# Kernel tuning notes

Hardware: AMD Instinct MI355X
Metric: run time of the kernel (lower is better)

The kernel has to match this reference:

```python
import jax, jax.numpy as jnp
import numpy as np

L = 16          # num transformer layers
D = 1024        # d_model
H = 16          # num heads
HD = 64         # head dim
LDIM = 512      # latent dim
TC = 512        # text conditioning length
PAST = 1024     # kv cache past length
FF = 4096       # ffn hidden
FH = 2048       # flow net hidden
MAX_PERIOD = 10000.0


def _ln(x, w, b, eps=1e-5):
    mu = jnp.mean(x, axis=-1, keepdims=True)
    var = jnp.mean((x - mu) ** 2, axis=-1, keepdims=True)
    return (x - mu) * jax.lax.rsqrt(var + eps) * w + b


def setup_inputs() -> dict:
    key = jax.random.key(0)
    ks = jax.random.split(key, 13)
    n = lambda k, s: jax.random.normal(k, s, dtype=jnp.float32)
    inp = {
        'text_embeddings': n(ks[0], (1, TC, D)),
        'prev_latent': n(ks[1], (1, 1, LDIM)),
        'kv_cache': n(ks[2], (L, 2, 1, PAST, H, HD)),
        'cache_len': PAST,
        'noise': n(ks[3], (1, LDIM)),
        'bos_emb': n(ks[4], (LDIM,)),
        'W_in': n(ks[5], (LDIM, D)) * 0.02, 'b_in': jnp.zeros((D,), jnp.float32),
        'ln1_w': jnp.ones((L, D), jnp.float32), 'ln1_b': jnp.zeros((L, D), jnp.float32),
        'Wqkv': n(ks[6], (L, D, 3 * D)) * 0.02, 'bqkv': jnp.zeros((L, 3 * D), jnp.float32),
        'Wo': n(ks[7], (L, D, D)) * 0.02, 'bo': jnp.zeros((L, D), jnp.float32),
        'ln2_w': jnp.ones((L, D), jnp.float32), 'ln2_b': jnp.zeros((L, D), jnp.float32),
        'W1': n(ks[8], (L, D, FF)) * 0.02, 'b1': jnp.zeros((L, FF), jnp.float32),
        'W2': n(ks[9], (L, FF, D)) * 0.02, 'b2': jnp.zeros((L, D), jnp.float32),
        'on_w': jnp.ones((D,), jnp.float32), 'on_b': jnp.zeros((D,), jnp.float32),
        'W_eos': n(ks[10], (D, 1)) * 0.02, 'b_eos': jnp.zeros((1,), jnp.float32),
        'Wf1': n(ks[11], (D + 2 + LDIM, FH)) * 0.02, 'bf1': jnp.zeros((FH,), jnp.float32),
        'Wf2': n(ks[12], (FH, LDIM)) * 0.02, 'bf2': jnp.zeros((LDIM,), jnp.float32),
    }
    return inp


def reference(text_embeddings, prev_latent, kv_cache, cache_len, noise, bos_emb,
              W_in, b_in, ln1_w, ln1_b, Wqkv, bqkv, Wo, bo, ln2_w, ln2_b,
              W1, b1, W2, b2, on_w, on_b, W_eos, b_eos, Wf1, bf1, Wf2, bf2):
    B = prev_latent.shape[0]
    prev = jnp.where(jnp.isnan(prev_latent), bos_emb[None, None, :], prev_latent)
    x = jnp.concatenate([text_embeddings, prev @ W_in + b_in], axis=1)  # [B,T,D]
    T = x.shape[1]
    Tkv = kv_cache.shape[3] + T

    # RoPE angles, shared across layers (offset = cache_len)
    half = HD // 2
    freqs = jnp.exp(jnp.arange(half, dtype=jnp.float32) * (-np.log(MAX_PERIOD) * 2.0 / HD))
    ts = jnp.arange(T, dtype=jnp.float32) + jnp.asarray(cache_len, jnp.float32)
    ang = ts[:, None] * freqs[None, :]               # [T, half]
    cos = jnp.cos(ang)[None, :, None, :]             # [1,T,1,half]
    sin = jnp.sin(ang)[None, :, None, :]

    # causal mask: new token q can see all past + itself
    mask = jnp.arange(Tkv)[None, :] <= (Tkv - T + jnp.arange(T)[:, None])  # [T,Tkv]
    scale = 1.0 / np.sqrt(HD)

    def rot(t):
        tr = t.reshape(B, T, H, half, 2)
        r, i = tr[..., 0], tr[..., 1]
        return jnp.stack([r * cos - i * sin, r * sin + i * cos], axis=-1).reshape(B, T, H, HD)

    def layer_fn(xc, p):
        l1w, l1b, wqkv, bq, wo, bo_, l2w, l2b, w1, b1_, w2, b2_, kv = p
        h = _ln(xc, l1w, l1b)
        qkv = (h @ wqkv + bq).reshape(B, T, 3, H, HD)
        q, k, v = qkv[:, :, 0], qkv[:, :, 1], qkv[:, :, 2]
        q, k = rot(q), rot(k)
        q = q.transpose(0, 2, 1, 3)                  # [B,H,T,HD]
        k = k.transpose(0, 2, 1, 3)
        v = v.transpose(0, 2, 1, 3)
        pk = kv[0].transpose(0, 2, 1, 3)             # [B,H,past,HD]
        pv = kv[1].transpose(0, 2, 1, 3)
        fk = jnp.concatenate([pk, k], axis=2)        # [B,H,Tkv,HD]
        fv = jnp.concatenate([pv, v], axis=2)
        scores = jnp.einsum('bhqd,bhkd->bhqk', q, fk) * scale
        scores = jnp.where(mask[None, None], scores, -1e30)
        attn = jax.nn.softmax(scores, axis=-1)
        o = jnp.einsum('bhqk,bhkd->bhqd', attn, fv).transpose(0, 2, 1, 3).reshape(B, T, D)
        xc = xc + o @ wo + bo_
        h2 = _ln(xc, l2w, l2b)
        xc = xc + jax.nn.gelu(h2 @ w1 + b1_, approximate=False) @ w2 + b2_
        new_kv = jnp.stack([fk.transpose(0, 2, 1, 3), fv.transpose(0, 2, 1, 3)])
        return xc, new_kv

    xs = (ln1_w, ln1_b, Wqkv, bqkv, Wo, bo, ln2_w, ln2_b, W1, b1, W2, b2, kv_cache)
    x, new_kv_cache = jax.lax.scan(layer_fn, x, xs)

    x = _ln(x.astype(jnp.float32), on_w, on_b)
    t_out = x[:, -1, :]                              # [B,D]
    is_eos = (t_out @ W_eos + b_eos) > -4.0
    s_time = jnp.zeros((B, 1), noise.dtype)
    t_time = jnp.ones((B, 1), noise.dtype)
    f_in = jnp.concatenate([t_out, s_time, t_time, noise], axis=-1)
    flow_dir = jax.nn.gelu(f_in @ Wf1 + bf1, approximate=False) @ Wf2 + bf2
    next_latent = noise + flow_dir
    new_cache_len = cache_len + T
    return next_latent, is_eos, new_kv_cache, new_cache_len
```

## Files before the change

kernel.cpp:

```cpp
#include <hip/hip_runtime.h>
#include <math.h>

#define KV_LS_STRIDE 1573888
#define KV_OUT_OFF 513
#define CLEN_OUT_IDX 50364929
#define VTP 1600

typedef __attribute__((ext_vector_type(8))) short short8;
typedef __attribute__((ext_vector_type(4))) short short4v;
typedef __attribute__((ext_vector_type(4))) float f32x4;

static __device__ __forceinline__ float gelu_f(float v){
  return 0.5f * v * (1.0f + erff(v * 0.70710678118654752f));
}
static __device__ __forceinline__ unsigned short f2b(float f){
  unsigned int u = __float_as_uint(f);
  u += 0x7fffu + ((u>>16)&1u);
  return (unsigned short)(u>>16);
}
__device__ __forceinline__ void gload16(const void* g, void* l){
  __builtin_amdgcn_global_load_lds((const __attribute__((address_space(1))) void*)g,
                                   (__attribute__((address_space(3))) void*)l, 16, 0, 0);
}

__global__ __launch_bounds__(256) void copy_past_k(const float* __restrict__ src,
                                                   float* __restrict__ dst){
  const long total = 16L*2*1024*1024;
  long stride = (long)gridDim.x * blockDim.x;
  for (long i = (long)blockIdx.x*blockDim.x + threadIdx.x; i < total; i += stride){
    long ls  = i >> 20;
    long rem = i & 1048575;
    dst[ls*KV_LS_STRIDE + rem] = src[i];
  }
}

__global__ __launch_bounds__(256) void copy_text_k(const float4* __restrict__ t,
                                                   float4* __restrict__ x){
  int i = blockIdx.x*256 + threadIdx.x;
  x[i] = t[i];
}

__global__ __launch_bounds__(256) void build512_k(const float* __restrict__ prev,
    const float* __restrict__ bos, const float* __restrict__ Win,
    const float* __restrict__ bin, float* __restrict__ x){
  __shared__ float red[16][17];
  int t = threadIdx.x;
  int n = blockIdx.x*16 + (t&15), ks = t>>4;
  float s = 0.f;
  for (int k=ks*32; k<ks*32+32; ++k){
    float p = prev[k];
    if (p != p) p = bos[k];
    s += p * Win[(size_t)k*1024 + n];
  }
  red[ks][t&15] = s;
  __syncthreads();
  if (t < 16){
    float acc = bin[blockIdx.x*16 + t];
    #pragma unroll
    for (int j=0;j<16;++j) acc += red[j][t];
    x[(size_t)512*1024 + blockIdx.x*16 + t] = acc;
  }
}

__global__ __launch_bounds__(256) void rope_tab_k(float* __restrict__ cost,
    float* __restrict__ sint, const int* __restrict__ clen){
  int i = blockIdx.x*256 + threadIdx.x;
  if (i >= 513*32) return;
  int t = i >> 5, j = i & 31;
  float freq = expf((float)j * (-0.28782313662425572f));
  float ang = (float)(t + clen[0]) * freq;
  cost[i] = cosf(ang);
  sint[i] = sinf(ang);
}

template<int BF16OUT>
__global__ __launch_bounds__(256) void ln_k(const float* __restrict__ x,
    const float* __restrict__ w, const float* __restrict__ b,
    float* __restrict__ outf, unsigned short* __restrict__ outh, int rows){
  int row = blockIdx.x; if (row >= rows) return;
  const float* xr = x + (size_t)row*1024;
  int tid = threadIdx.x;
  float4 v = *(const float4*)(xr + tid*4);
  float s  = v.x+v.y+v.z+v.w;
  float ss = v.x*v.x+v.y*v.y+v.z*v.z+v.w*v.w;
  for (int o=32;o;o>>=1){ s += __shfl_down(s,o); ss += __shfl_down(ss,o); }
  __shared__ float red[8];
  int wid = tid>>6;
  if ((tid&63)==0){ red[wid]=s; red[4+wid]=ss; }
  __syncthreads();
  if (tid==0){
    float ts = red[0]+red[1]+red[2]+red[3];
    float tss= red[4]+red[5]+red[6]+red[7];
    float mu = ts*(1.0f/1024.0f);
    float var= tss*(1.0f/1024.0f) - mu*mu;
    red[0]=mu; red[1]=rsqrtf(var + 1e-5f);
  }
  __syncthreads();
  float mu = red[0], rs = red[1];
  float4 wv = *(const float4*)(w + tid*4);
  float4 bv = *(const float4*)(b + tid*4);
  float4 o4;
  o4.x = (v.x-mu)*rs*wv.x + bv.x;
  o4.y = (v.y-mu)*rs*wv.y + bv.y;
  o4.z = (v.z-mu)*rs*wv.z + bv.z;
  o4.w = (v.w-mu)*rs*wv.w + bv.w;
  if (BF16OUT){
    uint2 u;
    u.x = (unsigned)f2b(o4.x) | ((unsigned)f2b(o4.y)<<16);
    u.y = (unsigned)f2b(o4.z) | ((unsigned)f2b(o4.w)<<16);
    *(uint2*)(outh + (size_t)row*1024 + tid*4) = u;
  } else {
    *(float4*)(outf + (size_t)row*1024 + tid*4) = o4;
  }
}

__global__ __launch_bounds__(256) void wtrans_k(const float* __restrict__ W,
    unsigned short* __restrict__ Wt, int K, int N){
  __shared__ float s[64][68];
  int t = threadIdx.x;
  int n0 = blockIdx.x*64, k0 = blockIdx.y*64;
  int r = t>>4, c4 = (t&15)<<2;
  #pragma unroll
  for (int p=0;p<4;++p){
    float4 v = *(const float4*)(W + (size_t)(k0 + r + p*16)*N + n0 + c4);
    *(float4*)&s[r + p*16][c4] = v;
  }
  __syncthreads();
  int n = t>>2, ks = t&3;
  unsigned short tmp[16];
  #pragma unroll
  for (int j=0;j<16;++j) tmp[j] = f2b(s[ks*16 + j][n]);
  size_t ob = (size_t)(n0+n)*K + k0 + ks*16;
  uint4 lo, hi;
  lo.x = tmp[0] | ((unsigned)tmp[1]<<16);  lo.y = tmp[2] | ((unsigned)tmp[3]<<16);
  lo.z = tmp[4] | ((unsigned)tmp[5]<<16);  lo.w = tmp[6] | ((unsigned)tmp[7]<<16);
  hi.x = tmp[8] | ((unsigned)tmp[9]<<16);  hi.y = tmp[10]| ((unsigned)tmp[11]<<16);
  hi.z = tmp[12]| ((unsigned)tmp[13]<<16); hi.w = tmp[14]| ((unsigned)tmp[15]<<16);
  *(uint4*)(Wt + ob)     = lo;
  *(uint4*)(Wt + ob + 8) = hi;
}

__global__ __launch_bounds__(256) void mgemm_k(const unsigned short* __restrict__ A,
    const unsigned short* __restrict__ Bt, float* __restrict__ P,
    int M, int N, int K, int kc){
  __shared__ unsigned short Alds[128*32];
  __shared__ unsigned short Blds[128*32];
  int tid = threadIdx.x;
  int w = tid>>6, l = tid&63;
  int m0 = blockIdx.y*128, n0 = blockIdx.x*128;
  int k0 = blockIdx.z*kc, k1 = k0+kc;
  f32x4 acc[4][4];
  #pragma unroll
  for (int i=0;i<4;++i)
    #pragma unroll
    for (int j=0;j<4;++j) acc[i][j] = (f32x4){0.f,0.f,0.f,0.f};
  const unsigned short* ga  = A  + (size_t)(m0 + w*32 + (l>>2))*K + (l&3)*8;
  const unsigned short* gbp = Bt + (size_t)(n0 + w*32 + (l>>2))*K + (l&3)*8;
  unsigned short* la = &Alds[(w*32)*32];
  unsigned short* lb = &Blds[(w*32)*32];
  int wr = w>>1, wc = w&1, lr = l&15, lg = l>>4;
  for (int k=k0; k<k1; k+=32){
    gload16(ga + k,                 &la[0]);
    gload16(ga + (size_t)16*K + k,  &la[16*32]);
    gload16(gbp + k,                &lb[0]);
    gload16(gbp + (size_t)16*K + k, &lb[16*32]);
    __syncthreads();
    short8 af[4], bfr[4];
    #pragma unroll
    for (int mi=0;mi<4;++mi)
      af[mi] = *(const short8*)&Alds[(wr*64 + mi*16 + lr)*32 + lg*8];
    #pragma unroll
    for (int ni=0;ni<4;++ni)
      bfr[ni] = *(const short8*)&Blds[(wc*64 + ni*16 + lr)*32 + lg*8];
    #pragma unroll
    for (int mi=0;mi<4;++mi)
      #pragma unroll
      for (int ni=0;ni<4;++ni)
        acc[mi][ni] = __builtin_amdgcn_mfma_f32_16x16x32_bf16(af[mi], bfr[ni], acc[mi][ni], 0, 0, 0);
    __syncthreads();
  }
  float* Pz = P + (size_t)blockIdx.z*M*N;
  #pragma unroll
  for (int mi=0;mi<4;++mi){
    int rb = m0 + wr*64 + mi*16 + lg*4;
    #pragma unroll
    for (int ni=0;ni<4;++ni){
      int col = n0 + wc*64 + ni*16 + lr;
      #pragma unroll
      for (int r=0;r<4;++r){
        int row = rb + r;
        if (row < M) Pz[(size_t)row*N + col] = acc[mi][ni][r];
      }
    }
  }
}

template<int KS, int MODE>
__global__ __launch_bounds__(256) void reduce_k(const float* __restrict__ P,
    const float* __restrict__ bias, float* __restrict__ outf,
    unsigned short* __restrict__ outh, int M, int N){
  int i = blockIdx.x*256 + threadIdx.x;
  int total = (M*N)>>2;
  if (i >= total) return;
  int col4 = (i % (N>>2))<<2;
  const float4* p4 = (const float4*)P;
  float4 s = p4[i];
  #pragma unroll
  for (int z=1; z<KS; ++z){
    float4 t = p4[i + (size_t)z*total];
    s.x+=t.x; s.y+=t.y; s.z+=t.z; s.w+=t.w;
  }
  float4 bv = *(const float4*)(bias + col4);
  s.x+=bv.x; s.y+=bv.y; s.z+=bv.z; s.w+=bv.w;
  if constexpr (MODE==0){
    ((float4*)outf)[i] = s;
  } else {
    uint2 u;
    u.x = (unsigned)f2b(gelu_f(s.x)) | ((unsigned)f2b(gelu_f(s.y))<<16);
    u.y = (unsigned)f2b(gelu_f(s.z)) | ((unsigned)f2b(gelu_f(s.w))<<16);
    ((uint2*)outh)[i] = u;
  }
}

template<int KS, int DOLN>
__global__ __launch_bounds__(256) void reduce_ln_k(const float* __restrict__ P,
    const float* __restrict__ bias, float* __restrict__ x,
    const float* __restrict__ lnw, const float* __restrict__ lnb,
    unsigned short* __restrict__ outh){
  const int M = 513;
  int row = blockIdx.x;
  int tid = threadIdx.x;
  int c4 = tid<<2;
  float4 sv = *(const float4*)(P + (size_t)row*1024 + c4);
  #pragma unroll
  for (int z=1; z<KS; ++z){
    float4 t = *(const float4*)(P + (size_t)z*M*1024 + (size_t)row*1024 + c4);
    sv.x+=t.x; sv.y+=t.y; sv.z+=t.z; sv.w+=t.w;
  }
  float4 bv = *(const float4*)(bias + c4);
  float4 xv = *(const float4*)(x + (size_t)row*1024 + c4);
  xv.x += sv.x+bv.x; xv.y += sv.y+bv.y; xv.z += sv.z+bv.z; xv.w += sv.w+bv.w;
  *(float4*)(x + (size_t)row*1024 + c4) = xv;
  if constexpr (DOLN){
    float s  = xv.x+xv.y+xv.z+xv.w;
    float ss = xv.x*xv.x+xv.y*xv.y+xv.z*xv.z+xv.w*xv.w;
    for (int o=32;o;o>>=1){ s += __shfl_down(s,o); ss += __shfl_down(ss,o); }
    __shared__ float red[8];
    int wid = tid>>6;
    if ((tid&63)==0){ red[wid]=s; red[4+wid]=ss; }
    __syncthreads();
    if (tid==0){
      float ts = red[0]+red[1]+red[2]+red[3];
      float tss= red[4]+red[5]+red[6]+red[7];
      float mu = ts*(1.0f/1024.0f);
      float var= tss*(1.0f/1024.0f) - mu*mu;
      red[0]=mu; red[1]=rsqrtf(var + 1e-5f);
    }
    __syncthreads();
    float mu = red[0], rs = red[1];
    float4 wv = *(const float4*)(lnw + c4);
    float4 bb = *(const float4*)(lnb + c4);
    float o0 = (xv.x-mu)*rs*wv.x + bb.x;
    float o1 = (xv.y-mu)*rs*wv.y + bb.y;
    float o2 = (xv.z-mu)*rs*wv.z + bb.z;
    float o3 = (xv.w-mu)*rs*wv.w + bb.w;
    uint2 u;
    u.x = (unsigned)f2b(o0) | ((unsigned)f2b(o1)<<16);
    u.y = (unsigned)f2b(o2) | ((unsigned)f2b(o3)<<16);
    *(uint2*)(outh + (size_t)row*1024 + c4) = u;
  }
}

__global__ __launch_bounds__(256) void past16_k(const float* __restrict__ kvK,
    const float* __restrict__ kvV, unsigned short* __restrict__ kb,
    unsigned short* __restrict__ vt){
  __shared__ float s[64][68];
  int hh = blockIdx.x, t0 = blockIdx.y*64;
  int tid = threadIdx.x;
  int row = tid>>4, c4 = (tid&15)<<2;
  #pragma unroll
  for (int p=0;p<4;++p){
    int rr = row + p*16;
    float4 v = *(const float4*)(kvK + (size_t)(t0+rr)*1024 + hh*64 + c4);
    uint2 u;
    u.x = (unsigned)f2b(v.x) | ((unsigned)f2b(v.y)<<16);
    u.y = (unsigned)f2b(v.z) | ((unsigned)f2b(v.w)<<16);
    *(uint2*)(kb + (size_t)(t0+rr)*1024 + hh*64 + c4) = u;
  }
  #pragma unroll
  for (int p=0;p<4;++p){
    int rr = row + p*16;
    float4 v = *(const float4*)(kvV + (size_t)(t0+rr)*1024 + hh*64 + c4);
    *(float4*)&s[rr][c4] = v;
  }
  __syncthreads();
  int n = tid>>2, ks = tid&3;
  unsigned short tmp[16];
  #pragma unroll
  for (int j=0;j<16;++j) tmp[j] = f2b(s[ks*16+j][n]);
  size_t ob = (size_t)(hh*64+n)*VTP + t0 + ks*16;
  uint4 lo, hi;
  lo.x = tmp[0] | ((unsigned)tmp[1]<<16);  lo.y = tmp[2] | ((unsigned)tmp[3]<<16);
  lo.z = tmp[4] | ((unsigned)tmp[5]<<16);  lo.w = tmp[6] | ((unsigned)tmp[7]<<16);
  hi.x = tmp[8] | ((unsigned)tmp[9]<<16);  hi.y = tmp[10]| ((unsigned)tmp[11]<<16);
  hi.z = tmp[12]| ((unsigned)tmp[13]<<16); hi.w = tmp[14]| ((unsigned)tmp[15]<<16);
  *(uint4*)(vt + ob)     = lo;
  *(uint4*)(vt + ob + 8) = hi;
}

__global__ __launch_bounds__(256) void qkv_post_k(const float* __restrict__ P,
    const float* __restrict__ bias, const float* __restrict__ cost,
    const float* __restrict__ sint, unsigned short* __restrict__ qb16,
    unsigned short* __restrict__ kb16, unsigned short* __restrict__ vt,
    float* __restrict__ kl, float* __restrict__ vl){
  __shared__ float s[64][68];
  const int M=513, N=3072;
  int hh = blockIdx.x, t0 = blockIdx.y*64;
  int tid = threadIdx.x;
  int row = tid>>4, c4 = (tid&15)<<2;
  #pragma unroll
  for (int p=0;p<4;++p){
    int rr = row + p*16;
    int t = t0 + rr;
    float4 vv = make_float4(0.f,0.f,0.f,0.f);
    if (t < M){
      const float* p0 = P + (size_t)t*N + hh*64 + c4;
      const float* p1 = p0 + (size_t)M*N;
      float4 a, b;
      a = *(const float4*)p0; b = *(const float4*)p1;
      float4 qv = make_float4(a.x+b.x, a.y+b.y, a.z+b.z, a.w+b.w);
      a = *(const float4*)(p0+1024); b = *(const float4*)(p1+1024);
      float4 kv = make_float4(a.x+b.x, a.y+b.y, a.z+b.z, a.w+b.w);
      a = *(const float4*)(p0+2048); b = *(const float4*)(p1+2048);
      vv = make_float4(a.x+b.x, a.y+b.y, a.z+b.z, a.w+b.w);
      float4 bq = *(const float4*)(bias + hh*64 + c4);
      float4 bk = *(const float4*)(bias + 1024 + hh*64 + c4);
      float4 bvv= *(const float4*)(bias + 2048 + hh*64 + c4);
      qv.x+=bq.x; qv.y+=bq.y; qv.z+=bq.z; qv.w+=bq.w;
      kv.x+=bk.x; kv.y+=bk.y; kv.z+=bk.z; kv.w+=bk.w;
      vv.x+=bvv.x; vv.y+=bvv.y; vv.z+=bvv.z; vv.w+=bvv.w;
      int jj = c4>>1;
      float c0 = cost[(t<<5)+jj],   s0 = sint[(t<<5)+jj];
      float c1 = cost[(t<<5)+jj+1], s1 = sint[(t<<5)+jj+1];
      float q0 = qv.x*c0 - qv.y*s0, q1 = qv.x*s0 + qv.y*c0;
      float q2 = qv.z*c1 - qv.w*s1, q3 = qv.z*s1 + qv.w*c1;
      float k0 = kv.x*c0 - kv.y*s0, k1 = kv.x*s0 + kv.y*c0;
      float k2 = kv.z*c1 - kv.w*s1, k3 = kv.z*s1 + kv.w*c1;
      uint2 uq;
      uq.x = (unsigned)f2b(q0) | ((unsigned)f2b(q1)<<16);
      uq.y = (unsigned)f2b(q2) | ((unsigned)f2b(q3)<<16);
      *(uint2*)(qb16 + (size_t)t*1024 + hh*64 + c4) = uq;
      uint2 uk;
      uk.x = (unsigned)f2b(k0) | ((unsigned)f2b(k1)<<16);
      uk.y = (unsigned)f2b(k2) | ((unsigned)f2b(k3)<<16);
      size_t ko = (size_t)(1024+t)*1024 + hh*64 + c4;
      *(uint2*)(kb16 + ko) = uk;
      kl[ko]=k0; kl[ko+1]=k1; kl[ko+2]=k2; kl[ko+3]=k3;
      vl[ko]=vv.x; vl[ko+1]=vv.y; vl[ko+2]=vv.z; vl[ko+3]=vv.w;
    }
    *(float4*)&s[rr][c4] = vv;
  }
  __syncthreads();
  int n = tid>>2, ks = tid&3;
  unsigned short tmp[16];
  #pragma unroll
  for (int j=0;j<16;++j) tmp[j] = f2b(s[ks*16+j][n]);
  size_t ob = (size_t)(hh*64+n)*VTP + 1024 + t0 + ks*16;
  uint4 lo, hi;
  lo.x = tmp[0] | ((unsigned)tmp[1]<<16);  lo.y = tmp[2] | ((unsigned)tmp[3]<<16);
  lo.z = tmp[4] | ((unsigned)tmp[5]<<16);  lo.w = tmp[6] | ((unsigned)tmp[7]<<16);
  hi.x = tmp[8] | ((unsigned)tmp[9]<<16);  hi.y = tmp[10]| ((unsigned)tmp[11]<<16);
  hi.z = tmp[12]| ((unsigned)tmp[13]<<16); hi.w = tmp[14]| ((unsigned)tmp[15]<<16);
  *(uint4*)(vt + ob)     = lo;
  *(uint4*)(vt + ob + 8) = hi;
}

static __device__ __forceinline__ f32x4 mfma32(short8 a, short8 b, f32x4 c){
  return __builtin_amdgcn_mfma_f32_16x16x32_bf16(a, b, c, 0, 0, 0);
}

__global__ __launch_bounds__(128) void attn_k(const unsigned short* __restrict__ qb,
    const unsigned short* __restrict__ kb, const unsigned short* __restrict__ vt,
    float* __restrict__ Oc, float* __restrict__ ml){
  const int T=513, Tkv=1537, past=1024;
  int hh = blockIdx.x, bt = blockIdx.y, ch = blockIdx.z;
  int wv = threadIdx.x >> 6, l = threadIdx.x & 63;
  int g = l >> 4, lr = l & 15;
  int q0 = bt*32 + wv*16;
  int gq = q0 + lr;
  const unsigned short* qp = qb + (size_t)gq*1024 + hh*64 + g*8;
  short8 qf0 = *(const short8*)qp;
  short8 qf1 = *(const short8*)(qp+32);
  f32x4 acc_o[4];
  #pragma unroll
  for (int i=0;i<4;++i) acc_o[i] = (f32x4){0.f,0.f,0.f,0.f};
  float m_run = -1e30f, l_run = 0.f;
  int kend_w = past + q0 + 16; if (kend_w > Tkv) kend_w = Tkv;
  int kstart = ch*384;
  int kend = (ch==3) ? kend_w : ((ch+1)*384 < kend_w ? (ch+1)*384 : kend_w);
  const float scale = 0.125f;
  for (int kt0 = kstart; kt0 < kend; kt0 += 64){
    float p[16];
    #pragma unroll
    for (int st=0; st<4; ++st){
      const unsigned short* kp = kb + (size_t)(kt0+st*16+lr)*1024 + hh*64 + g*8;
      short8 kf0 = *(const short8*)kp;
      short8 kf1 = *(const short8*)(kp+32);
      f32x4 s4 = (f32x4){0.f,0.f,0.f,0.f};
      s4 = mfma32(kf0, qf0, s4);
      s4 = mfma32(kf1, qf1, s4);
      #pragma unroll
      for (int r=0;r<4;++r) p[st*4+r] = s4[r]*scale;
    }
    if (kt0 + 63 > past + q0 + 15 || kt0 + 63 >= Tkv){
      #pragma unroll
      for (int st=0; st<4; ++st)
        #pragma unroll
        for (int r=0;r<4;++r){
          int kt = kt0 + st*16 + g*4 + r;
          if (kt > past + gq || kt >= Tkv) p[st*4+r] = -1e30f;
        }
    }
    float tmax = p[0];
    #pragma unroll
    for (int i=1;i<16;++i) tmax = fmaxf(tmax, p[i]);
    tmax = fmaxf(tmax, __shfl_xor(tmax,16));
    tmax = fmaxf(tmax, __shfl_xor(tmax,32));
    float m_new = fmaxf(m_run, tmax);
    float sc = __expf(m_run - m_new);
    float psum = 0.f;
    #pragma unroll
    for (int i=0;i<16;++i){ p[i] = __expf(p[i] - m_new); psum += p[i]; }
    psum += __shfl_xor(psum,16); psum += __shfl_xor(psum,32);
    l_run = l_run*sc + psum;
    m_run = m_new;
    #pragma unroll
    for (int db=0;db<4;++db){
      acc_o[db][0]*=sc; acc_o[db][1]*=sc; acc_o[db][2]*=sc; acc_o[db][3]*=sc;
    }
    short8 pf[4];
    #pragma unroll
    for (int st=0; st<4; ++st){
      union { short8 s8; unsigned int u[4]; } pu;
      pu.u[0] = (unsigned)f2b(p[st*4+0]) | ((unsigned)f2b(p[st*4+1])<<16);
      pu.u[1] = (unsigned)f2b(p[st*4+2]) | ((unsigned)f2b(p[st*4+3])<<16);
      pu.u[2] = 0; pu.u[3] = 0;
      pf[st] = pu.s8;
    }
    #pragma unroll
    for (int st=0; st<4; ++st){
      #pragma unroll
      for (int db=0; db<4; ++db){
        const unsigned short* vp = vt + (size_t)(hh*64 + db*16 + lr)*VTP + kt0 + st*16 + g*4;
        short4v v4 = *(const short4v*)vp;
        short8 va = (short8){v4[0],v4[1],v4[2],v4[3],0,0,0,0};
        acc_o[db] = mfma32(va, pf[st], acc_o[db]);
      }
    }
  }
  if (gq < T){
    size_t ob = ((size_t)(ch*16+hh)*544 + gq)*64;
    #pragma unroll
    for (int db=0;db<4;++db)
      *(float4*)(Oc + ob + db*16 + g*4) = make_float4(acc_o[db][0],acc_o[db][1],acc_o[db][2],acc_o[db][3]);
    if (g==0){
      size_t mo = ((size_t)(ch*16+hh)*544 + gq)*2;
      ml[mo] = m_run; ml[mo+1] = l_run;
    }
  }
}

__global__ __launch_bounds__(256) void attn_comb_k(const float* __restrict__ Oc,
    const float* __restrict__ ml, unsigned short* __restrict__ obb){
  int qg = blockIdx.x;
  int t = threadIdx.x;
  int hh = t>>4, d4 = (t&15)<<2;
  float m[4], lv[4];
  float mm = -1e30f;
  #pragma unroll
  for (int c=0;c<4;++c){
    size_t mo = ((size_t)(c*16+hh)*544 + qg)*2;
    m[c]=ml[mo]; lv[c]=ml[mo+1];
    mm = fmaxf(mm, m[c]);
  }
  float w[4], denom = 0.f;
  #pragma unroll
  for (int c=0;c<4;++c){ w[c] = __expf(m[c]-mm); denom += lv[c]*w[c]; }
  float inv = 1.0f/denom;
  float r0=0.f,r1=0.f,r2=0.f,r3=0.f;
  #pragma unroll
  for (int c=0;c<4;++c){
    float4 o = *(const float4*)(Oc + (((size_t)(c*16+hh)*544+qg)*64 + d4));
    r0 += o.x*w[c]; r1 += o.y*w[c]; r2 += o.z*w[c]; r3 += o.w*w[c];
  }
  r0*=inv; r1*=inv; r2*=inv; r3*=inv;
  uint2 u;
  u.x = (unsigned)f2b(r0) | ((unsigned)f2b(r1)<<16);
  u.y = (unsigned)f2b(r2) | ((unsigned)f2b(r3)<<16);
  *(uint2*)(obb + (size_t)qg*1024 + hh*64 + d4) = u;
}

__global__ __launch_bounds__(256) void eos_tail_k(const float* __restrict__ tout,
    const float* __restrict__ Weos, const float* __restrict__ beos,
    const int* __restrict__ clen, float* __restrict__ out){
  int tid = threadIdx.x;
  float s = 0.f;
  for (int i=tid;i<1024;i+=256) s += tout[i]*Weos[i];
  for (int o=32;o;o>>=1) s += __shfl_down(s,o);
  __shared__ float red[4];
  if ((tid&63)==0) red[tid>>6] = s;
  __syncthreads();
  if (tid==0){
    float v = red[0]+red[1]+red[2]+red[3] + beos[0];
    out[512] = (v > -4.0f) ? 1.0f : 0.0f;
    out[CLEN_OUT_IDX] = (float)(clen[0] + 513);
  }
}

__global__ __launch_bounds__(256) void flow1_k(const float* __restrict__ tout,
    const float* __restrict__ noise, const float* __restrict__ Wf1,
    const float* __restrict__ bf1, float* __restrict__ fh){
  __shared__ float red[16][17];
  int t = threadIdx.x;
  int n = blockIdx.x*16 + (t&15), ks = t>>4;
  float s = 0.f;
  for (int k=ks*96; k<ks*96+96; ++k){
    float in = (k < 1024) ? tout[k] : noise[k-1024];
    size_t krow = (k < 1024) ? (size_t)k : (size_t)(k+2);
    s += in * Wf1[krow*2048 + n];
  }
  red[ks][t&15] = s;
  __syncthreads();
  if (t < 16){
    int nn = blockIdx.x*16 + t;
    float acc = bf1[nn] + Wf1[(size_t)1025*2048 + nn];
    #pragma unroll
    for (int j=0;j<16;++j) acc += red[j][t];
    fh[nn] = gelu_f(acc);
  }
}

__global__ __launch_bounds__(256) void flow2_k(const float* __restrict__ fh,
    const float* __restrict__ noise, const float* __restrict__ Wf2,
    const float* __restrict__ bf2, float* __restrict__ out){
  __shared__ float red[16][17];
  int t = threadIdx.x;
  int n = blockIdx.x*16 + (t&15), ks = t>>4;
  float s = 0.f;
  for (int k=ks*128; k<ks*128+128; ++k) s += fh[k]*Wf2[(size_t)k*512 + n];
  red[ks][t&15] = s;
  __syncthreads();
  if (t < 16){
    int nn = blockIdx.x*16 + t;
    float acc = bf2[nn];
    #pragma unroll
    for (int j=0;j<16;++j) acc += red[j][t];
    out[nn] = noise[nn] + acc;
  }
}

extern "C" void kernel_launch(void* const* d_in, const int* in_sizes, int n_in,
                              void* d_out, int out_size, void* d_ws, size_t ws_size,
                              hipStream_t stream) {
  const float* text  = (const float*)d_in[0];
  const float* prevl = (const float*)d_in[1];
  const float* kvin  = (const float*)d_in[2];
  const int*   clen  = (const int*)  d_in[3];
  const float* noise = (const float*)d_in[4];
  const float* bos   = (const float*)d_in[5];
  const float* Win   = (const float*)d_in[6];
  const float* bin   = (const float*)d_in[7];
  const float* ln1w  = (const float*)d_in[8];
  const float* ln1b  = (const float*)d_in[9];
  const float* Wqkv  = (const float*)d_in[10];
  const float* bqkv  = (const float*)d_in[11];
  const float* Wo    = (const float*)d_in[12];
  const float* bo    = (const float*)d_in[13];
  const float* ln2w  = (const float*)d_in[14];
  const float* ln2b  = (const float*)d_in[15];
  const float* W1    = (const float*)d_in[16];
  const float* b1    = (const float*)d_in[17];
  const float* W2    = (const float*)d_in[18];
  const float* b2    = (const float*)d_in[19];
  const float* onw   = (const float*)d_in[20];
  const float* onb   = (const float*)d_in[21];
  const float* Weos  = (const float*)d_in[22];
  const float* beos  = (const float*)d_in[23];
  const float* Wf1   = (const float*)d_in[24];
  const float* bf1   = (const float*)d_in[25];
  const float* Wf2   = (const float*)d_in[26];
  const float* bf2   = (const float*)d_in[27];

  float* out   = (float*)d_out;
  float* kvout = out + KV_OUT_OFF;
  float* ws = (float*)d_ws;
  float* x    = ws;
  float* Pbuf = x    + 525312;
  float* Oc   = Pbuf + 4202496;
  float* mlb  = Oc   + 2228224;
  float* cost = mlb  + 69632;
  float* sint = cost + 16416;
  float* tout = sint + 16416;
  float* fh   = tout + 1024;
  unsigned short* hb   = (unsigned short*)(fh + 2048);
  unsigned short* gb   = hb   + 655360;
  unsigned short* obb  = gb   + 2621440;
  unsigned short* qb16 = obb  + 655360;
  unsigned short* kb16 = qb16 + 557056;
  unsigned short* vt16 = kb16 + 1638400;
  unsigned short* qkvT = vt16 + 1638400;
  unsigned short* woT  = qkvT + 3145728;
  unsigned short* w1T  = woT  + 1048576;
  unsigned short* w2T  = w1T  + 4194304;

  copy_past_k<<<4096,256,0,stream>>>(kvin, kvout);
  copy_text_k<<<512,256,0,stream>>>((const float4*)text, (float4*)x);
  build512_k<<<64,256,0,stream>>>(prevl, bos, Win, bin, x);
  rope_tab_k<<<65,256,0,stream>>>(cost, sint, clen);
  ln_k<1><<<513,256,0,stream>>>(x, ln1w, ln1b, nullptr, hb, 513);

  for (int l=0; l<16; ++l){
    float* kl = kvout + (size_t)(2*l)  *KV_LS_STRIDE;
    float* vl = kvout + (size_t)(2*l+1)*KV_LS_STRIDE;
    const float* kvK = kvin + (size_t)l*2*1024*1024;
    const float* kvV = kvK + 1024*1024;
    past16_k<<<dim3(16,16),256,0,stream>>>(kvK, kvV, kb16, vt16);
    wtrans_k<<<dim3(48,16),256,0,stream>>>(Wqkv+(size_t)l*1024*3072, qkvT, 1024, 3072);
    mgemm_k<<<dim3(24,5,2),256,0,stream>>>(hb, qkvT, Pbuf, 513, 3072, 1024, 512);
    qkv_post_k<<<dim3(16,9),256,0,stream>>>(Pbuf, bqkv+(size_t)l*3072, cost, sint,
        qb16, kb16, vt16, kl, vl);
    attn_k<<<dim3(16,17,4),128,0,stream>>>(qb16, kb16, vt16, Oc, mlb);
    attn_comb_k<<<513,256,0,stream>>>(Oc, mlb, obb);
    wtrans_k<<<dim3(16,16),256,0,stream>>>(Wo+(size_t)l*1024*1024, woT, 1024, 1024);
    mgemm_k<<<dim3(8,5,4),256,0,stream>>>(obb, woT, Pbuf, 513, 1024, 1024, 256);
    reduce_ln_k<4,1><<<513,256,0,stream>>>(Pbuf, bo+(size_t)l*1024, x,
        ln2w+(size_t)l*1024, ln2b+(size_t)l*1024, hb);
    wtrans_k<<<dim3(64,16),256,0,stream>>>(W1+(size_t)l*1024*4096, w1T, 1024, 4096);
    mgemm_k<<<dim3(32,5,2),256,0,stream>>>(hb, w1T, Pbuf, 513, 4096, 1024, 512);
    reduce_k<2,2><<<2052,256,0,stream>>>(Pbuf, b1+(size_t)l*4096, nullptr, gb, 513, 4096);
    wtrans_k<<<dim3(16,64),256,0,stream>>>(W2+(size_t)l*4096*1024, w2T, 4096, 1024);
    mgemm_k<<<dim3(8,5,8),256,0,stream>>>(gb, w2T, Pbuf, 513, 1024, 4096, 512);
    if (l < 15)
      reduce_ln_k<8,1><<<513,256,0,stream>>>(Pbuf, b2+(size_t)l*1024, x,
          ln1w+(size_t)(l+1)*1024, ln1b+(size_t)(l+1)*1024, hb);
    else
      reduce_ln_k<8,0><<<513,256,0,stream>>>(Pbuf, b2+(size_t)l*1024, x,
          nullptr, nullptr, nullptr);
  }

  ln_k<0><<<1,256,0,stream>>>(x + (size_t)512*1024, onw, onb, tout, nullptr, 1);
  eos_tail_k<<<1,256,0,stream>>>(tout, Weos, beos, clen, out);
  flow1_k<<<128,256,0,stream>>>(tout, noise, Wf1, bf1, fh);
  flow2_k<<<32,256,0,stream>>>(fh, noise, Wf2, bf2, out);
}
```

Before: 2.634 ms.

## Batch weight transposes and KV conversion for all layers up front, fuse past-KV copy

Moves the per-layer bf16 weight transposes and past-KV conversion into a few large batched launches before the layer loop, using per-layer workspace slices. The past-KV output copy is folded into past16_k, so the separate copy kernel goes away. The W2 GEMM split-K factor also drops from 8 to 4, with the matching reduce. This cuts kernel count and turns small, poorly occupied per-layer launches into large ones, at the cost of a much bigger workspace. The fused kernel writes the KV output with scalar stores instead of vector stores.

```diff
diff --git a/kernel.cpp b/kernel.cpp
--- a/kernel.cpp
+++ b/kernel.cpp
@@ -5,6 +5,7 @@
 #define KV_OUT_OFF 513
 #define CLEN_OUT_IDX 50364929
 #define VTP 1600
+#define KVL 1638400
 
 typedef __attribute__((ext_vector_type(8))) short short8;
 typedef __attribute__((ext_vector_type(4))) short short4v;
@@ -21,17 +22,6 @@
 __device__ __forceinline__ void gload16(const void* g, void* l){
   __builtin_amdgcn_global_load_lds((const __attribute__((address_space(1))) void*)g,
                                    (__attribute__((address_space(3))) void*)l, 16, 0, 0);
-}
-
-__global__ __launch_bounds__(256) void copy_past_k(const float* __restrict__ src,
-                                                   float* __restrict__ dst){
-  const long total = 16L*2*1024*1024;
-  long stride = (long)gridDim.x * blockDim.x;
-  for (long i = (long)blockIdx.x*blockDim.x + threadIdx.x; i < total; i += stride){
-    long ls  = i >> 20;
-    long rem = i & 1048575;
-    dst[ls*KV_LS_STRIDE + rem] = src[i];
-  }
 }
 
 __global__ __launch_bounds__(256) void copy_text_k(const float4* __restrict__ t,
@@ -117,6 +107,9 @@
 __global__ __launch_bounds__(256) void wtrans_k(const float* __restrict__ W,
     unsigned short* __restrict__ Wt, int K, int N){
   __shared__ float s[64][68];
+  int l = blockIdx.z;
+  W  += (size_t)l*K*N;
+  Wt += (size_t)l*N*K;
   int t = threadIdx.x;
   int n0 = blockIdx.x*64, k0 = blockIdx.y*64;
   int r = t>>4, c4 = (t&15)<<2;
@@ -271,27 +264,33 @@
   }
 }
 
-__global__ __launch_bounds__(256) void past16_k(const float* __restrict__ kvK,
-    const float* __restrict__ kvV, unsigned short* __restrict__ kb,
-    unsigned short* __restrict__ vt){
+__global__ __launch_bounds__(256) void past16_k(const float* __restrict__ kvin,
+    unsigned short* __restrict__ kb, unsigned short* __restrict__ vt,
+    float* __restrict__ kvout){
   __shared__ float s[64][68];
+  int l = blockIdx.z;
   int hh = blockIdx.x, t0 = blockIdx.y*64;
+  const float* kvK = kvin + (size_t)l*2097152;
+  const float* kvV = kvK + 1048576;
+  unsigned short* kbL = kb + (size_t)l*KVL;
+  unsigned short* vtL = vt + (size_t)l*KVL;
+  float* kl = kvout + (size_t)(2*l)  *KV_LS_STRIDE;
+  float* vl = kvout + (size_t)(2*l+1)*KV_LS_STRIDE;
   int tid = threadIdx.x;
   int row = tid>>4, c4 = (tid&15)<<2;
   #pragma unroll
   for (int p=0;p<4;++p){
     int rr = row + p*16;
-    float4 v = *(const float4*)(kvK + (size_t)(t0+rr)*1024 + hh*64 + c4);
+    size_t off = (size_t)(t0+rr)*1024 + hh*64 + c4;
+    float4 v = *(const float4*)(kvK + off);
     uint2 u;
     u.x = (unsigned)f2b(v.x) | ((unsigned)f2b(v.y)<<16);
     u.y = (unsigned)f2b(v.z) | ((unsigned)f2b(v.w)<<16);
-    *(uint2*)(kb + (size_t)(t0+rr)*1024 + hh*64 + c4) = u;
-  }
-  #pragma unroll
-  for (int p=0;p<4;++p){
-    int rr = row + p*16;
-    float4 v = *(const float4*)(kvV + (size_t)(t0+rr)*1024 + hh*64 + c4);
-    *(float4*)&s[rr][c4] = v;
+    *(uint2*)(kbL + off) = u;
+    kl[off]=v.x; kl[off+1]=v.y; kl[off+2]=v.z; kl[off+3]=v.w;
+    float4 w = *(const float4*)(kvV + off);
+    *(float4*)&s[rr][c4] = w;
+    vl[off]=w.x; vl[off+1]=w.y; vl[off+2]=w.z; vl[off+3]=w.w;
   }
   __syncthreads();
   int n = tid>>2, ks = tid&3;
@@ -304,8 +303,8 @@
   lo.z = tmp[4] | ((unsigned)tmp[5]<<16);  lo.w = tmp[6] | ((unsigned)tmp[7]<<16);
   hi.x = tmp[8] | ((unsigned)tmp[9]<<16);  hi.y = tmp[10]| ((unsigned)tmp[11]<<16);
   hi.z = tmp[12]| ((unsigned)tmp[13]<<16); hi.w = tmp[14]| ((unsigned)tmp[15]<<16);
-  *(uint4*)(vt + ob)     = lo;
-  *(uint4*)(vt + ob + 8) = hi;
+  *(uint4*)(vtL + ob)     = lo;
+  *(uint4*)(vtL + ob + 8) = hi;
 }
 
 __global__ __launch_bounds__(256) void qkv_post_k(const float* __restrict__ P,
@@ -607,13 +606,17 @@
   unsigned short* obb  = gb   + 2621440;
   unsigned short* qb16 = obb  + 655360;
   unsigned short* kb16 = qb16 + 557056;
-  unsigned short* vt16 = kb16 + 1638400;
-  unsigned short* qkvT = vt16 + 1638400;
-  unsigned short* woT  = qkvT + 3145728;
-  unsigned short* w1T  = woT  + 1048576;
-  unsigned short* w2T  = w1T  + 4194304;
-
-  copy_past_k<<<4096,256,0,stream>>>(kvin, kvout);
+  unsigned short* vt16 = kb16 + (size_t)16*KVL;
+  unsigned short* qkvT = vt16 + (size_t)16*KVL;
+  unsigned short* woT  = qkvT + (size_t)16*3145728;
+  unsigned short* w1T  = woT  + (size_t)16*1048576;
+  unsigned short* w2T  = w1T  + (size_t)16*4194304;
+
+  past16_k<<<dim3(16,16,16),256,0,stream>>>(kvin, kb16, vt16, kvout);
+  wtrans_k<<<dim3(48,16,16),256,0,stream>>>(Wqkv, qkvT, 1024, 3072);
+  wtrans_k<<<dim3(16,16,16),256,0,stream>>>(Wo,   woT,  1024, 1024);
+  wtrans_k<<<dim3(64,16,16),256,0,stream>>>(W1,   w1T,  1024, 4096);
+  wtrans_k<<<dim3(16,64,16),256,0,stream>>>(W2,   w2T,  4096, 1024);
   copy_text_k<<<512,256,0,stream>>>((const float4*)text, (float4*)x);
   build512_k<<<64,256,0,stream>>>(prevl, bos, Win, bin, x);
   rope_tab_k<<<65,256,0,stream>>>(cost, sint, clen);
@@ -622,29 +625,24 @@
   for (int l=0; l<16; ++l){
     float* kl = kvout + (size_t)(2*l)  *KV_LS_STRIDE;
     float* vl = kvout + (size_t)(2*l+1)*KV_LS_STRIDE;
-    const float* kvK = kvin + (size_t)l*2*1024*1024;
-    const float* kvV = kvK + 1024*1024;
-    past16_k<<<dim3(16,16),256,0,stream>>>(kvK, kvV, kb16, vt16);
-    wtrans_k<<<dim3(48,16),256,0,stream>>>(Wqkv+(size_t)l*1024*3072, qkvT, 1024, 3072);
-    mgemm_k<<<dim3(24,5,2),256,0,stream>>>(hb, qkvT, Pbuf, 513, 3072, 1024, 512);
+    unsigned short* kbL = kb16 + (size_t)l*KVL;
+    unsigned short* vtL = vt16 + (size_t)l*KVL;
+    mgemm_k<<<dim3(24,5,2),256,0,stream>>>(hb, qkvT+(size_t)l*3145728, Pbuf, 513, 3072, 1024, 512);
     qkv_post_k<<<dim3(16,9),256,0,stream>>>(Pbuf, bqkv+(size_t)l*3072, cost, sint,
-        qb16, kb16, vt16, kl, vl);
-    attn_k<<<dim3(16,17,4),128,0,stream>>>(qb16, kb16, vt16, Oc, mlb);
+        qb16, kbL, vtL, kl, vl);
+    attn_k<<<dim3(16,17,4),128,0,stream>>>(qb16, kbL, vtL, Oc, mlb);
     attn_comb_k<<<513,256,0,stream>>>(Oc, mlb, obb);
-    wtrans_k<<<dim3(16,16),256,0,stream>>>(Wo+(size_t)l*1024*1024, woT, 1024, 1024);
-    mgemm_k<<<dim3(8,5,4),256,0,stream>>>(obb, woT, Pbuf, 513, 1024, 1024, 256);
+    mgemm_k<<<dim3(8,5,4),256,0,stream>>>(obb, woT+(size_t)l*1048576, Pbuf, 513, 1024, 1024, 256);
     reduce_ln_k<4,1><<<513,256,0,stream>>>(Pbuf, bo+(size_t)l*1024, x,
         ln2w+(size_t)l*1024, ln2b+(size_t)l*1024, hb);
-    wtrans_k<<<dim3(64,16),256,0,stream>>>(W1+(size_t)l*1024*4096, w1T, 1024, 4096);
-    mgemm_k<<<dim3(32,5,2),256,0,stream>>>(hb, w1T, Pbuf, 513, 4096, 1024, 512);
+    mgemm_k<<<dim3(32,5,2),256,0,stream>>>(hb, w1T+(size_t)l*4194304, Pbuf, 513, 4096, 1024, 512);
     reduce_k<2,2><<<2052,256,0,stream>>>(Pbuf, b1+(size_t)l*4096, nullptr, gb, 513, 4096);
-    wtrans_k<<<dim3(16,64),256,0,stream>>>(W2+(size_t)l*4096*1024, w2T, 4096, 1024);
-    mgemm_k<<<dim3(8,5,8),256,0,stream>>>(gb, w2T, Pbuf, 513, 1024, 4096, 512);
+    mgemm_k<<<dim3(8,5,4),256,0,stream>>>(gb, w2T+(size_t)l*4194304, Pbuf, 513, 1024, 4096, 1024);
     if (l < 15)
-      reduce_ln_k<8,1><<<513,256,0,stream>>>(Pbuf, b2+(size_t)l*1024, x,
+      reduce_ln_k<4,1><<<513,256,0,stream>>>(Pbuf, b2+(size_t)l*1024, x,
           ln1w+(size_t)(l+1)*1024, ln1b+(size_t)(l+1)*1024, hb);
     else
-      reduce_ln_k<8,0><<<513,256,0,stream>>>(Pbuf, b2+(size_t)l*1024, x,
+      reduce_ln_k<4,0><<<513,256,0,stream>>>(Pbuf, b2+(size_t)l*1024, x,
           nullptr, nullptr, nullptr);
   }
 
```

New measurement: 2.763 ms. +4.9%, slower.
